# Optimization experiments

Hardware: AMD Instinct MI355X
Metric: run time of the kernel (lower is better)

The kernel has to match this reference:

```python
import jax, jax.numpy as jnp
import numpy as np

N_BOOK = 16  # == len_code; C() loop is only consistent when len_code == n_book


def setup_inputs() -> dict:
    key = jax.random.key(0)
    k1, k2 = jax.random.split(key)
    N = 32768
    D = 256        # len_code * n_book = 16 * 16
    n_classes = 4096
    features = jax.random.normal(k1, (N, D), dtype=jnp.float32)
    # Prototypes passed transposed relative to storage: [len_code*n_book, n_classes]
    Prototypes = jax.random.normal(k2, (D, n_classes), dtype=jnp.float32)
    return {"features": features, "Prototypes": Prototypes}


def reference(features, Prototypes):
    # Faithful to GPQSoftMaxNet.C: per-book matmul, concat over books, mean.
    # features: [N, len_code*n_book] split along dim 1 into chunks of width n_book
    # Prototypes: [len_code*n_book, n_classes] split along dim 0 into chunks of height n_book
    n_book = N_BOOK
    N, D = features.shape
    n_classes = Prototypes.shape[1]
    f = features.reshape(N, -1, n_book)          # [N, n_book(=len_code), n_book]
    P = Prototypes.reshape(-1, n_book, n_classes)  # [n_book(=len_code), n_book, n_classes]
    # mean over books of per-book GEMMs, fused into one einsum (no [N,C,n_book] intermediate)
    logits = jnp.einsum('nbd,bdc->nc', f, P) / jnp.float32(n_book)
    return logits
```

## Files before the change

### kernel.cpp

```cpp
#include <hip/hip_runtime.h>
#include <hip/hip_bf16.h>

typedef __attribute__((ext_vector_type(8))) short short8;
typedef __attribute__((ext_vector_type(4))) float f32x4;

static constexpr int MT = 32768;
static constexpr int KT = 256;
static constexpr int CT = 4096;

__device__ __forceinline__ unsigned short f2b(float f) {
  unsigned int b = __float_as_uint(f);
  b += 0x7FFFu + ((b >> 16) & 1u);
  return (unsigned short)(b >> 16);
}

__global__ void __launch_bounds__(256) cvtA_kernel(const float* __restrict__ A,
                                                   unsigned short* __restrict__ Abf) {
  int i = blockIdx.x * 256 + threadIdx.x;
  const float4 v0 = reinterpret_cast<const float4*>(A)[2 * i];
  const float4 v1 = reinterpret_cast<const float4*>(A)[2 * i + 1];
  short8 o;
  o[0] = (short)f2b(v0.x); o[1] = (short)f2b(v0.y);
  o[2] = (short)f2b(v0.z); o[3] = (short)f2b(v0.w);
  o[4] = (short)f2b(v1.x); o[5] = (short)f2b(v1.y);
  o[6] = (short)f2b(v1.z); o[7] = (short)f2b(v1.w);
  reinterpret_cast<short8*>(Abf)[i] = o;
}

__global__ void __launch_bounds__(1024) cvtB_kernel(const float* __restrict__ B,
                                                    unsigned short* __restrict__ Bt) {
  __shared__ unsigned short tile[32][33];
  int tx = threadIdx.x & 31, ty = threadIdx.x >> 5;
  int c0 = blockIdx.x * 32, k0 = blockIdx.y * 32;
  tile[ty][tx] = f2b(B[(size_t)(k0 + ty) * CT + c0 + tx]);
  __syncthreads();
  Bt[(size_t)(c0 + ty) * KT + k0 + tx] = tile[tx][ty];
}

__device__ __forceinline__ void gload16(const void* g, void* l) {
  __builtin_amdgcn_global_load_lds(
      (const __attribute__((address_space(1))) void*)g,
      (__attribute__((address_space(3))) void*)l, 16, 0, 0);
}

__global__ void __launch_bounds__(256) gemm_kernel(const unsigned short* __restrict__ Abf,
                                                   const unsigned short* __restrict__ Btw,
                                                   float* __restrict__ O) {
  constexpr int BM = 128, BN = 128, BK = 32;
  __shared__ __align__(16) char smem[32 * 132 * 4];
  unsigned short* Al = (unsigned short*)smem;
  unsigned short* Bl = (unsigned short*)(smem + 8192);
  float* eb = (float*)smem;

  int bid = blockIdx.x;
  int wg = (bid & 7) * (8192 / 8) + (bid >> 3);
  int tc = wg & 31;
  int tr = wg >> 5;
  int r0 = tr * BM, c0 = tc * BN;

  int tid = threadIdx.x;
  int lane = tid & 63, wid = tid >> 6;
  int wr = wid >> 1, wc = wid & 1;
  int l15 = lane & 15, l4 = lane >> 4;

  f32x4 acc[4][4] = {};

  const int rowA = tid >> 2;
  const int kofs = (tid & 3) * 8;

  for (int t = 0; t < KT / BK; ++t) {
    if (t) __syncthreads();
#pragma unroll
    for (int j = 0; j < 2; ++j) {
      gload16(Abf + (size_t)(r0 + j * 64 + rowA) * KT + t * BK + kofs,
              Al + j * 2048 + wid * 512);
      gload16(Btw + (size_t)(c0 + j * 64 + rowA) * KT + t * BK + kofs,
              Bl + j * 2048 + wid * 512);
    }
    __syncthreads();

    short8 af[4], bf[4];
#pragma unroll
    for (int m = 0; m < 4; ++m)
      af[m] = *reinterpret_cast<const short8*>(Al + (wr * 64 + m * 16 + l15) * BK + l4 * 8);
#pragma unroll
    for (int n = 0; n < 4; ++n)
      bf[n] = *reinterpret_cast<const short8*>(Bl + (wc * 64 + n * 16 + l15) * BK + l4 * 8);
#pragma unroll
    for (int n = 0; n < 4; ++n)
#pragma unroll
      for (int m = 0; m < 4; ++m)
        acc[n][m] = __builtin_amdgcn_mfma_f32_16x16x32_bf16(bf[n], af[m], acc[n][m], 0, 0, 0);
  }

  const float s = 1.0f / 16.0f;
#pragma unroll
  for (int m = 0; m < 4; ++m) {
    __syncthreads();
#pragma unroll
    for (int n = 0; n < 4; ++n) {
      f32x4 v = acc[n][m];
      v[0] *= s; v[1] *= s; v[2] *= s; v[3] *= s;
      int lrow = wr * 16 + l15;
      int col = wc * 64 + n * 16 + l4 * 4;
      *reinterpret_cast<f32x4*>(&eb[lrow * 132 + col]) = v;
    }
    __syncthreads();
#pragma unroll
    for (int p = 0; p < 4; ++p) {
      int r = p * 8 + (tid >> 5);
      int chunk = tid & 31;
      f32x4 v = *reinterpret_cast<const f32x4*>(&eb[r * 132 + chunk * 4]);
      int grow = (r >> 4) * 64 + m * 16 + (r & 15);
      __builtin_nontemporal_store(v, reinterpret_cast<f32x4*>(
          O + (size_t)(r0 + grow) * CT + c0 + chunk * 4));
    }
  }
}

__global__ void __launch_bounds__(256) naive_kernel(const float* __restrict__ A,
                                                    const float* __restrict__ B,
                                                    float* __restrict__ O) {
  size_t i = (size_t)blockIdx.x * 256 + threadIdx.x;
  int col = (int)(i & (size_t)(CT - 1));
  int row = (int)(i >> 12);
  float s = 0.f;
  for (int k = 0; k < KT; ++k)
    s += A[(size_t)row * KT + k] * B[(size_t)k * CT + col];
  O[i] = s * (1.0f / 16.0f);
}

extern "C" void kernel_launch(void* const* d_in, const int* in_sizes, int n_in,
                              void* d_out, int out_size, void* d_ws, size_t ws_size,
                              hipStream_t stream) {
  const float* A = (const float*)d_in[0];
  const float* B = (const float*)d_in[1];
  float* O = (float*)d_out;
  const size_t needA = (size_t)MT * KT * sizeof(unsigned short);
  const size_t needB = (size_t)CT * KT * sizeof(unsigned short);
  if (ws_size >= needA + needB) {
    unsigned short* Abf = (unsigned short*)d_ws;
    unsigned short* Btw = (unsigned short*)((char*)d_ws + needA);
    cvtA_kernel<<<MT * KT / 8 / 256, 256, 0, stream>>>(A, Abf);
    cvtB_kernel<<<dim3(CT / 32, KT / 32), 1024, 0, stream>>>(B, Btw);
    gemm_kernel<<<(MT / 128) * (CT / 128), 256, 0, stream>>>(Abf, Btw, O);
  } else {
    naive_kernel<<<(unsigned)((size_t)MT * CT / 256), 256, 0, stream>>>(A, B, O);
  }
}
```

Before: 141.5 us.

## Retile GEMM to 32x256 blocks and merge conversion kernels into one launch

Switches the bf16 MFMA GEMM from 128x128 to 32x256 output tiles. Each wave computes 16x128 with one A fragment and eight B fragments, and the epilogue becomes a single LDS-staged pass writing full 1KB rows. It also fuses the A conversion and B transpose-convert into one launch with 256-thread blocks. This is meant to cut launch overhead and streamline the store-dominated epilogue, at the cost of less operand reuse per block and more B re-reads.

```diff
diff --git a/kernel.cpp b/kernel.cpp
--- a/kernel.cpp
+++ b/kernel.cpp
@@ -14,27 +14,38 @@
   return (unsigned short)(b >> 16);
 }
 
-__global__ void __launch_bounds__(256) cvtA_kernel(const float* __restrict__ A,
-                                                   unsigned short* __restrict__ Abf) {
-  int i = blockIdx.x * 256 + threadIdx.x;
-  const float4 v0 = reinterpret_cast<const float4*>(A)[2 * i];
-  const float4 v1 = reinterpret_cast<const float4*>(A)[2 * i + 1];
-  short8 o;
-  o[0] = (short)f2b(v0.x); o[1] = (short)f2b(v0.y);
-  o[2] = (short)f2b(v0.z); o[3] = (short)f2b(v0.w);
-  o[4] = (short)f2b(v1.x); o[5] = (short)f2b(v1.y);
-  o[6] = (short)f2b(v1.z); o[7] = (short)f2b(v1.w);
-  reinterpret_cast<short8*>(Abf)[i] = o;
-}
-
-__global__ void __launch_bounds__(1024) cvtB_kernel(const float* __restrict__ B,
-                                                    unsigned short* __restrict__ Bt) {
+__global__ void __launch_bounds__(256) cvt_kernel(const float* __restrict__ A,
+                                                  const float* __restrict__ B,
+                                                  unsigned short* __restrict__ Abf,
+                                                  unsigned short* __restrict__ Bt) {
   __shared__ unsigned short tile[32][33];
-  int tx = threadIdx.x & 31, ty = threadIdx.x >> 5;
-  int c0 = blockIdx.x * 32, k0 = blockIdx.y * 32;
-  tile[ty][tx] = f2b(B[(size_t)(k0 + ty) * CT + c0 + tx]);
-  __syncthreads();
-  Bt[(size_t)(c0 + ty) * KT + k0 + tx] = tile[tx][ty];
+  int bid = blockIdx.x, tid = threadIdx.x;
+  if (bid < 4096) {
+    int i = bid * 256 + tid;
+    const float4 v0 = reinterpret_cast<const float4*>(A)[2 * i];
+    const float4 v1 = reinterpret_cast<const float4*>(A)[2 * i + 1];
+    short8 o;
+    o[0] = (short)f2b(v0.x); o[1] = (short)f2b(v0.y);
+    o[2] = (short)f2b(v0.z); o[3] = (short)f2b(v0.w);
+    o[4] = (short)f2b(v1.x); o[5] = (short)f2b(v1.y);
+    o[6] = (short)f2b(v1.z); o[7] = (short)f2b(v1.w);
+    reinterpret_cast<short8*>(Abf)[i] = o;
+  } else {
+    int b = bid - 4096;
+    int c0 = (b & 127) * 32, k0 = (b >> 7) * 32;
+    int tx = tid & 31, ty0 = tid >> 5;
+#pragma unroll
+    for (int i = 0; i < 4; ++i) {
+      int ty = ty0 + i * 8;
+      tile[ty][tx] = f2b(B[(size_t)(k0 + ty) * CT + c0 + tx]);
+    }
+    __syncthreads();
+#pragma unroll
+    for (int i = 0; i < 4; ++i) {
+      int cy = ty0 + i * 8;
+      Bt[(size_t)(c0 + cy) * KT + k0 + tx] = tile[tx][cy];
+    }
+  }
 }
 
 __device__ __forceinline__ void gload16(const void* g, void* l) {
@@ -46,16 +57,16 @@
 __global__ void __launch_bounds__(256) gemm_kernel(const unsigned short* __restrict__ Abf,
                                                    const unsigned short* __restrict__ Btw,
                                                    float* __restrict__ O) {
-  constexpr int BM = 128, BN = 128, BK = 32;
-  __shared__ __align__(16) char smem[32 * 132 * 4];
+  constexpr int BM = 32, BN = 256, BK = 32;
+  __shared__ __align__(16) char smem[32 * 264 * 4];
   unsigned short* Al = (unsigned short*)smem;
-  unsigned short* Bl = (unsigned short*)(smem + 8192);
+  unsigned short* Bl = (unsigned short*)(smem + 2048);
   float* eb = (float*)smem;
 
   int bid = blockIdx.x;
-  int wg = (bid & 7) * (8192 / 8) + (bid >> 3);
-  int tc = wg & 31;
-  int tr = wg >> 5;
+  int wg = (bid & 7) * 2048 + (bid >> 3);
+  int tc = wg & 15;
+  int tr = wg >> 4;
   int r0 = tr * BM, c0 = tc * BN;
 
   int tid = threadIdx.x;
@@ -63,58 +74,46 @@
   int wr = wid >> 1, wc = wid & 1;
   int l15 = lane & 15, l4 = lane >> 4;
 
-  f32x4 acc[4][4] = {};
+  f32x4 acc[8] = {};
 
-  const int rowA = tid >> 2;
-  const int kofs = (tid & 3) * 8;
+  const int rowL = lane >> 2;
+  const int kofs = (lane & 3) * 8;
 
   for (int t = 0; t < KT / BK; ++t) {
     if (t) __syncthreads();
+    if (wid < 2)
+      gload16(Abf + (size_t)(r0 + wid * 16 + rowL) * KT + t * BK + kofs,
+              Al + wid * 512);
 #pragma unroll
-    for (int j = 0; j < 2; ++j) {
-      gload16(Abf + (size_t)(r0 + j * 64 + rowA) * KT + t * BK + kofs,
-              Al + j * 2048 + wid * 512);
-      gload16(Btw + (size_t)(c0 + j * 64 + rowA) * KT + t * BK + kofs,
-              Bl + j * 2048 + wid * 512);
-    }
+    for (int i = 0; i < 4; ++i)
+      gload16(Btw + (size_t)(c0 + i * 64 + wid * 16 + rowL) * KT + t * BK + kofs,
+              Bl + (i * 64 + wid * 16) * 32);
     __syncthreads();
 
-    short8 af[4], bf[4];
+    short8 af = *reinterpret_cast<const short8*>(Al + (wr * 16 + l15) * 32 + l4 * 8);
 #pragma unroll
-    for (int m = 0; m < 4; ++m)
-      af[m] = *reinterpret_cast<const short8*>(Al + (wr * 64 + m * 16 + l15) * BK + l4 * 8);
-#pragma unroll
-    for (int n = 0; n < 4; ++n)
-      bf[n] = *reinterpret_cast<const short8*>(Bl + (wc * 64 + n * 16 + l15) * BK + l4 * 8);
-#pragma unroll
-    for (int n = 0; n < 4; ++n)
-#pragma unroll
-      for (int m = 0; m < 4; ++m)
-        acc[n][m] = __builtin_amdgcn_mfma_f32_16x16x32_bf16(bf[n], af[m], acc[n][m], 0, 0, 0);
+    for (int n = 0; n < 8; ++n) {
+      short8 bf = *reinterpret_cast<const short8*>(
+          Bl + (wc * 128 + n * 16 + l15) * 32 + l4 * 8);
+      acc[n] = __builtin_amdgcn_mfma_f32_16x16x32_bf16(bf, af, acc[n], 0, 0, 0);
+    }
   }
 
   const float s = 1.0f / 16.0f;
+  __syncthreads();
 #pragma unroll
-  for (int m = 0; m < 4; ++m) {
-    __syncthreads();
+  for (int n = 0; n < 8; ++n) {
+    f32x4 v = acc[n];
+    v[0] *= s; v[1] *= s; v[2] *= s; v[3] *= s;
+    *reinterpret_cast<f32x4*>(&eb[(wr * 16 + l15) * 264 + wc * 128 + n * 16 + l4 * 4]) = v;
+  }
+  __syncthreads();
 #pragma unroll
-    for (int n = 0; n < 4; ++n) {
-      f32x4 v = acc[n][m];
-      v[0] *= s; v[1] *= s; v[2] *= s; v[3] *= s;
-      int lrow = wr * 16 + l15;
-      int col = wc * 64 + n * 16 + l4 * 4;
-      *reinterpret_cast<f32x4*>(&eb[lrow * 132 + col]) = v;
-    }
-    __syncthreads();
-#pragma unroll
-    for (int p = 0; p < 4; ++p) {
-      int r = p * 8 + (tid >> 5);
-      int chunk = tid & 31;
-      f32x4 v = *reinterpret_cast<const f32x4*>(&eb[r * 132 + chunk * 4]);
-      int grow = (r >> 4) * 64 + m * 16 + (r & 15);
-      __builtin_nontemporal_store(v, reinterpret_cast<f32x4*>(
-          O + (size_t)(r0 + grow) * CT + c0 + chunk * 4));
-    }
+  for (int p = 0; p < 8; ++p) {
+    int r = p * 4 + wid;
+    f32x4 v = *reinterpret_cast<const f32x4*>(&eb[r * 264 + lane * 4]);
+    __builtin_nontemporal_store(v, reinterpret_cast<f32x4*>(
+        O + (size_t)(r0 + r) * CT + c0 + lane * 4));
   }
 }
 
@@ -141,9 +140,8 @@
   if (ws_size >= needA + needB) {
     unsigned short* Abf = (unsigned short*)d_ws;
     unsigned short* Btw = (unsigned short*)((char*)d_ws + needA);
-    cvtA_kernel<<<MT * KT / 8 / 256, 256, 0, stream>>>(A, Abf);
-    cvtB_kernel<<<dim3(CT / 32, KT / 32), 1024, 0, stream>>>(B, Btw);
-    gemm_kernel<<<(MT / 128) * (CT / 128), 256, 0, stream>>>(Abf, Btw, O);
+    cvt_kernel<<<4096 + 1024, 256, 0, stream>>>(A, B, Abf, Btw);
+    gemm_kernel<<<(MT / 32) * (CT / 256), 256, 0, stream>>>(Abf, Btw, O);
   } else {
     naive_kernel<<<(unsigned)((size_t)MT * CT / 256), 256, 0, stream>>>(A, B, O);
   }
```

Measured after the change: 193.7 us. 1.37x slower.
